# Kernel optimization log

Hardware: AMD Instinct MI355X
Metric: run time of the kernel (lower is better)

## Reference

```python
import jax, jax.numpy as jnp
import numpy as np

D_MODEL = 1024
N_HEAD = 16
HEAD_DIM = D_MODEL // N_HEAD
BS, SEQ = 4, 2048
NEG_INF = -1e9


def setup_inputs() -> dict:
    key = jax.random.key(0)
    ks = jax.random.split(key, 10)
    X = jax.random.normal(ks[0], (BS, SEQ, D_MODEL), dtype=jnp.float32)
    kpm = jax.random.randint(ks[1], (BS, SEQ), 0, 2, dtype=jnp.int32)
    kpm = kpm.at[:, 0].set(0)  # guarantee at least one attendable key per batch
    scale = 1.0 / np.sqrt(D_MODEL)
    WQ = jax.random.normal(ks[2], (D_MODEL, D_MODEL), dtype=jnp.float32) * scale
    bQ = jnp.zeros((D_MODEL,), dtype=jnp.float32)
    WK = jax.random.normal(ks[3], (D_MODEL, D_MODEL), dtype=jnp.float32) * scale
    bK = jnp.zeros((D_MODEL,), dtype=jnp.float32)
    WV = jax.random.normal(ks[4], (D_MODEL, D_MODEL), dtype=jnp.float32) * scale
    bV = jnp.zeros((D_MODEL,), dtype=jnp.float32)
    WO = jax.random.normal(ks[5], (D_MODEL, D_MODEL), dtype=jnp.float32) * scale
    bO = jnp.zeros((D_MODEL,), dtype=jnp.float32)
    return {"X": X, "key_padding_mask": kpm, "WQ": WQ, "bQ": bQ,
            "WK": WK, "bK": bK, "WV": WV, "bV": bV, "WO": WO, "bO": bO}


def reference(X, key_padding_mask, WQ, bQ, WK, bK, WV, bV, WO, bO):
    bs, L, _ = X.shape
    # separate Q/K/V linear projections (torch Linear: x @ W.T + b)
    Q = X @ WQ.T + bQ
    K = X @ WK.T + bK
    V = X @ WV.T + bV
    # split heads: (bs, L, H, Dh) -> (bs, H, L, Dh)
    Q = Q.reshape(bs, L, N_HEAD, HEAD_DIM).transpose(0, 2, 1, 3)
    K = K.reshape(bs, L, N_HEAD, HEAD_DIM).transpose(0, 2, 1, 3)
    V = V.reshape(bs, L, N_HEAD, HEAD_DIM).transpose(0, 2, 1, 3)
    # scaled dot-product attention
    scores = jnp.einsum('bhqd,bhkd->bhqk', Q, K) / jnp.sqrt(
        jnp.asarray(HEAD_DIM, dtype=Q.dtype))
    # key padding mask: non-zero => ignore that key
    mask = (key_padding_mask != 0)[:, None, None, :]  # (bs,1,1,L)
    scores = jnp.where(mask, NEG_INF, scores)
    attn = jax.nn.softmax(scores, axis=-1)
    out = jnp.einsum('bhqk,bhkd->bhqd', attn, V)
    # merge heads
    out = out.transpose(0, 2, 1, 3).reshape(bs, L, D_MODEL)
    return out @ WO.T + bO
```

## Files before the change

kernel.cpp:

```cpp
#include <hip/hip_runtime.h>
#include <stdint.h>

#define BS_   4
#define SEQ_  2048
#define DM_   1024
#define NH_   16
#define DH_   64
#define MTOK_ (BS_*SEQ_)

typedef __attribute__((ext_vector_type(8))) short bf16x8;
typedef __attribute__((ext_vector_type(4))) float f32x4;

__device__ __forceinline__ unsigned short f2bf(float f) {
    union { float f; uint32_t u; } v; v.f = f;
    uint32_t r = v.u + 0x7fffu + ((v.u >> 16) & 1u);
    return (unsigned short)(r >> 16);
}

__device__ __forceinline__ float fexp2(float x) {
#if __has_builtin(__builtin_amdgcn_exp2f)
    return __builtin_amdgcn_exp2f(x);
#else
    return __expf(x * 0.69314718055994531f);
#endif
}

__device__ __forceinline__ uint32_t cvt_pk_bf16(float lo, float hi) {
    uint32_t r;
    asm("v_cvt_pk_bf16_f32 %0, %1, %2" : "=v"(r) : "v"(lo), "v"(hi));
    return r;
}

__device__ __forceinline__ void gload_lds16(const void* g, void* l) {
    __builtin_amdgcn_global_load_lds(
        (const __attribute__((address_space(1))) void*)g,
        (__attribute__((address_space(3))) void*)l, 16, 0, 0);
}

__global__ void cvt_kernel(const float* __restrict__ src,
                           unsigned short* __restrict__ dst, int n) {
    int i = (blockIdx.x * blockDim.x + threadIdx.x) * 4;
    const int stride = gridDim.x * blockDim.x * 4;
    for (; i < n; i += stride) {
        float4 v = *(const float4*)(src + i);
        ushort4 o;
        o.x = f2bf(v.x); o.y = f2bf(v.y); o.z = f2bf(v.z); o.w = f2bf(v.w);
        *(ushort4*)(dst + i) = o;
    }
}

template<int MODE>
__global__ __launch_bounds__(256) void gemm_bt(
    const unsigned short* __restrict__ A,
    const unsigned short* __restrict__ B,
    int Ndim, int Kdim,
    const float* __restrict__ bias0,
    const float* __restrict__ bias1,
    const float* __restrict__ bias2,
    unsigned short* __restrict__ Qo,
    unsigned short* __restrict__ Ko,
    unsigned short* __restrict__ Vt,
    float* __restrict__ Co)
{
    __shared__ unsigned short As[128 * 32];
    __shared__ unsigned short Bs[128 * 32];

    const int t    = threadIdx.x;
    const int lane = t & 63;
    const int w    = t >> 6;
    const int wr   = w >> 1, wc = w & 1;
    const int g    = lane >> 4, li = lane & 15;

    const int ntile = Ndim >> 7;
    const int tm = blockIdx.x / ntile;
    const int tn = blockIdx.x % ntile;

    const unsigned short* Ab = A + (size_t)tm * 128 * Kdim;
    const unsigned short* Bb = B + (size_t)tn * 128 * Kdim;

    f32x4 acc[4][4];
    const f32x4 zero = {0.f, 0.f, 0.f, 0.f};
    #pragma unroll
    for (int i = 0; i < 4; ++i)
        #pragma unroll
        for (int j = 0; j < 4; ++j)
            acc[i][j] = zero;

    const int s0 = t, s1 = t + 256;
    const int r0 = s0 >> 2, c0 = (s0 & 3) << 3;
    const int r1 = s1 >> 2, c1 = (s1 & 3) << 3;

    for (int k0 = 0; k0 < Kdim; k0 += 32) {
        gload_lds16(Ab + (size_t)r0 * Kdim + k0 + c0, (char*)As + s0 * 16);
        gload_lds16(Ab + (size_t)r1 * Kdim + k0 + c1, (char*)As + s1 * 16);
        gload_lds16(Bb + (size_t)r0 * Kdim + k0 + c0, (char*)Bs + s0 * 16);
        gload_lds16(Bb + (size_t)r1 * Kdim + k0 + c1, (char*)Bs + s1 * 16);
        __syncthreads();

        bf16x8 a[4], b[4];
        #pragma unroll
        for (int mi = 0; mi < 4; ++mi)
            a[mi] = *(const bf16x8*)&As[(wr * 64 + mi * 16 + li) * 32 + g * 8];
        #pragma unroll
        for (int ni = 0; ni < 4; ++ni)
            b[ni] = *(const bf16x8*)&Bs[(wc * 64 + ni * 16 + li) * 32 + g * 8];

        #pragma unroll
        for (int mi = 0; mi < 4; ++mi)
            #pragma unroll
            for (int ni = 0; ni < 4; ++ni)
                acc[mi][ni] = __builtin_amdgcn_mfma_f32_16x16x32_bf16(
                    a[mi], b[ni], acc[mi][ni], 0, 0, 0);
        __syncthreads();
    }

    if constexpr (MODE == 0) {
        #pragma unroll
        for (int mi = 0; mi < 4; ++mi) {
            const int gm0 = tm * 128 + wr * 64 + mi * 16 + g * 4;
            const int bb  = gm0 >> 11;
            const int l0  = gm0 & (SEQ_ - 1);
            #pragma unroll
            for (int ni = 0; ni < 4; ++ni) {
                const int gn  = tn * 128 + wc * 64 + ni * 16 + li;
                const int mat = gn >> 10;
                const int c   = gn & (DM_ - 1);
                const int hh  = c >> 6;
                const int dd  = c & (DH_ - 1);
                const float bias = (mat == 0 ? bias0 : (mat == 1 ? bias1 : bias2))[c];
                const f32x4 v = acc[mi][ni];
                if (mat == 2) {
                    ushort4 o;
                    o.x = f2bf(v[0] + bias);
                    o.y = f2bf(v[1] + bias);
                    o.z = f2bf(v[2] + bias);
                    o.w = f2bf(v[3] + bias);
                    *(ushort4*)&Vt[((size_t)(bb * NH_ + hh) * DH_ + dd) * SEQ_ + l0] = o;
                } else {
                    unsigned short* dst = (mat == 0) ? Qo : Ko;
                    #pragma unroll
                    for (int r = 0; r < 4; ++r)
                        dst[((size_t)(bb * NH_ + hh) * SEQ_ + l0 + r) * DH_ + dd] =
                            f2bf(v[r] + bias);
                }
            }
        }
    } else {
        #pragma unroll
        for (int mi = 0; mi < 4; ++mi) {
            const int gm0 = tm * 128 + wr * 64 + mi * 16 + g * 4;
            #pragma unroll
            for (int ni = 0; ni < 4; ++ni) {
                const int gn = tn * 128 + wc * 64 + ni * 16 + li;
                const float bias = bias0[gn];
                #pragma unroll
                for (int r = 0; r < 4; ++r)
                    Co[(size_t)(gm0 + r) * Ndim + gn] = acc[mi][ni][r] + bias;
            }
        }
    }
}

#define KPAD 72

__global__ __launch_bounds__(256) void attn_kernel(
    const unsigned short* __restrict__ Q,
    const unsigned short* __restrict__ K,
    const unsigned short* __restrict__ Vt,
    const int* __restrict__ kpm,
    unsigned short* __restrict__ Oo)
{
    __shared__ unsigned short Ks[64 * KPAD];
    __shared__ unsigned short Vs[64 * KPAD];
    __shared__ float maskLds[64];

    const int t    = threadIdx.x;
    const int lane = t & 63;
    const int w    = t >> 6;
    const int g    = lane >> 4, li = lane & 15;

    const int bh = blockIdx.x >> 4;
    const int qt = blockIdx.x & 15;
    const int b  = bh >> 4;
    const int h  = bh & 15;
    const int q0 = qt * 128 + w * 32;

    bf16x8 qf[2][2];
    #pragma unroll
    for (int qi = 0; qi < 2; ++qi)
        #pragma unroll
        for (int kk = 0; kk < 2; ++kk)
            qf[qi][kk] = *(const bf16x8*)&Q[((size_t)bh * SEQ_ + q0 + qi * 16 + li) * DH_
                                            + kk * 32 + g * 8];

    f32x4 Oacc[2][4];
    const f32x4 zero = {0.f, 0.f, 0.f, 0.f};
    #pragma unroll
    for (int qi = 0; qi < 2; ++qi)
        #pragma unroll
        for (int di = 0; di < 4; ++di)
            Oacc[qi][di] = zero;

    float mrun[2] = {-1e30f, -1e30f};
    float lrun[2] = {0.f, 0.f};

    const int sr = t >> 3;
    const int sc = (t & 7) * 8;

    bf16x8 kreg0, kreg1, vreg0, vreg1;
    float mreg = 0.f;

    auto load_tile = [&](int kv) {
        kreg0 = *(const bf16x8*)&K[((size_t)bh * SEQ_ + kv + sr) * DH_ + sc];
        kreg1 = *(const bf16x8*)&K[((size_t)bh * SEQ_ + kv + sr + 32) * DH_ + sc];
        vreg0 = *(const bf16x8*)&Vt[((size_t)bh * DH_ + sr) * SEQ_ + kv + sc];
        vreg1 = *(const bf16x8*)&Vt[((size_t)bh * DH_ + sr + 32) * SEQ_ + kv + sc];
        if (t < 64) mreg = kpm[b * SEQ_ + kv + t] ? -1e9f : 0.0f;
    };
    auto store_tile = [&]() {
        *(bf16x8*)&Ks[sr * KPAD + sc] = kreg0;
        *(bf16x8*)&Ks[(sr + 32) * KPAD + sc] = kreg1;
        *(bf16x8*)&Vs[sr * KPAD + sc] = vreg0;
        *(bf16x8*)&Vs[(sr + 32) * KPAD + sc] = vreg1;
        if (t < 64) maskLds[t] = mreg;
    };

    load_tile(0);
    store_tile();

    const float SA = 0.18033688011112042f;

    for (int kv = 0; kv < SEQ_; kv += 64) {
        __syncthreads();
        const bool more = (kv + 64) < SEQ_;
        if (more) load_tile(kv + 64);

        float4 mk[4];
        #pragma unroll
        for (int ni = 0; ni < 4; ++ni)
            mk[ni] = *(const float4*)&maskLds[ni * 16 + g * 4];

        f32x4 sacc[2][4];
        #pragma unroll
        for (int qi = 0; qi < 2; ++qi)
            #pragma unroll
            for (int ni = 0; ni < 4; ++ni)
                sacc[qi][ni] = zero;
        #pragma unroll
        for (int ni = 0; ni < 4; ++ni) {
            #pragma unroll
            for (int kk = 0; kk < 2; ++kk) {
                bf16x8 kb = *(const bf16x8*)&Ks[(ni * 16 + li) * KPAD + kk * 32 + g * 8];
                sacc[0][ni] = __builtin_amdgcn_mfma_f32_16x16x32_bf16(
                    kb, qf[0][kk], sacc[0][ni], 0, 0, 0);
                sacc[1][ni] = __builtin_amdgcn_mfma_f32_16x16x32_bf16(
                    kb, qf[1][kk], sacc[1][ni], 0, 0, 0);
            }
        }

        #pragma unroll
        for (int qi = 0; qi < 2; ++qi)
            #pragma unroll
            for (int ni = 0; ni < 4; ++ni) {
                sacc[qi][ni][0] = sacc[qi][ni][0] * SA + mk[ni].x;
                sacc[qi][ni][1] = sacc[qi][ni][1] * SA + mk[ni].y;
                sacc[qi][ni][2] = sacc[qi][ni][2] * SA + mk[ni].z;
                sacc[qi][ni][3] = sacc[qi][ni][3] * SA + mk[ni].w;
            }

        #pragma unroll
        for (int qi = 0; qi < 2; ++qi) {
            float pm = sacc[qi][0][0];
            #pragma unroll
            for (int ni = 0; ni < 4; ++ni)
                #pragma unroll
                for (int r = 0; r < 4; ++r)
                    pm = fmaxf(pm, sacc[qi][ni][r]);
            pm = fmaxf(pm, __shfl_xor(pm, 16));
            pm = fmaxf(pm, __shfl_xor(pm, 32));
            if (!__all(pm <= mrun[qi] + 8.0f)) {
                const float mnew = fmaxf(mrun[qi], pm);
                const float scl  = fexp2(mrun[qi] - mnew);
                mrun[qi] = mnew;
                lrun[qi] *= scl;
                #pragma unroll
                for (int di = 0; di < 4; ++di)
                    #pragma unroll
                    for (int r = 0; r < 4; ++r)
                        Oacc[qi][di][r] *= scl;
            }
            float rs = 0.f;
            #pragma unroll
            for (int ni = 0; ni < 4; ++ni)
                #pragma unroll
                for (int r = 0; r < 4; ++r) {
                    const float p = fexp2(sacc[qi][ni][r] - mrun[qi]);
                    sacc[qi][ni][r] = p;
                    rs += p;
                }
            rs += __shfl_xor(rs, 16);
            rs += __shfl_xor(rs, 32);
            lrun[qi] += rs;
        }

        bf16x8 pa[2][2];
        #pragma unroll
        for (int qi = 0; qi < 2; ++qi)
            #pragma unroll
            for (int kk = 0; kk < 2; ++kk) {
                union { bf16x8 v; uint32_t w4[4]; } u;
                u.w4[0] = cvt_pk_bf16(sacc[qi][2 * kk][0],     sacc[qi][2 * kk][1]);
                u.w4[1] = cvt_pk_bf16(sacc[qi][2 * kk][2],     sacc[qi][2 * kk][3]);
                u.w4[2] = cvt_pk_bf16(sacc[qi][2 * kk + 1][0], sacc[qi][2 * kk + 1][1]);
                u.w4[3] = cvt_pk_bf16(sacc[qi][2 * kk + 1][2], sacc[qi][2 * kk + 1][3]);
                pa[qi][kk] = u.v;
            }

        #pragma unroll
        for (int di = 0; di < 4; ++di) {
            #pragma unroll
            for (int kk = 0; kk < 2; ++kk) {
                union { bf16x8 v; ushort4 h[2]; } uv;
                uv.h[0] = *(const ushort4*)&Vs[(di * 16 + li) * KPAD + kk * 32 + g * 4];
                uv.h[1] = *(const ushort4*)&Vs[(di * 16 + li) * KPAD + kk * 32 + 16 + g * 4];
                Oacc[0][di] = __builtin_amdgcn_mfma_f32_16x16x32_bf16(
                    uv.v, pa[0][kk], Oacc[0][di], 0, 0, 0);
                Oacc[1][di] = __builtin_amdgcn_mfma_f32_16x16x32_bf16(
                    uv.v, pa[1][kk], Oacc[1][di], 0, 0, 0);
            }
        }

        __syncthreads();
        if (more) store_tile();
    }

    #pragma unroll
    for (int qi = 0; qi < 2; ++qi) {
        const float inv = 1.0f / lrun[qi];
        const int q = q0 + qi * 16 + li;
        #pragma unroll
        for (int di = 0; di < 4; ++di) {
            ushort4 o;
            o.x = f2bf(Oacc[qi][di][0] * inv);
            o.y = f2bf(Oacc[qi][di][1] * inv);
            o.z = f2bf(Oacc[qi][di][2] * inv);
            o.w = f2bf(Oacc[qi][di][3] * inv);
            *(ushort4*)&Oo[((size_t)b * SEQ_ + q) * DM_ + h * 64 + di * 16 + g * 4] = o;
        }
    }
}

extern "C" void kernel_launch(void* const* d_in, const int* in_sizes, int n_in,
                              void* d_out, int out_size, void* d_ws, size_t ws_size,
                              hipStream_t stream) {
    const float* X  = (const float*)d_in[0];
    const int*  kpm = (const int*)d_in[1];
    const float* WQ = (const float*)d_in[2];
    const float* bQ = (const float*)d_in[3];
    const float* WK = (const float*)d_in[4];
    const float* bK = (const float*)d_in[5];
    const float* WV = (const float*)d_in[6];
    const float* bV = (const float*)d_in[7];
    const float* WO = (const float*)d_in[8];
    const float* bO = (const float*)d_in[9];
    float* Out = (float*)d_out;

    char* ws = (char*)d_ws;
    unsigned short* Xb  = (unsigned short*)(ws);
    unsigned short* Wb  = (unsigned short*)(ws + (16u << 20));
    unsigned short* WOb = (unsigned short*)(ws + (22u << 20));
    unsigned short* Qb  = (unsigned short*)(ws + (24u << 20));
    unsigned short* Kb  = (unsigned short*)(ws + (40u << 20));
    unsigned short* Vtb = (unsigned short*)(ws + (56u << 20));
    unsigned short* AOb = Xb;

    cvt_kernel<<<2048, 256, 0, stream>>>(X,  Xb,                 (int)(MTOK_ * DM_));
    cvt_kernel<<<1024, 256, 0, stream>>>(WQ, Wb,                 DM_ * DM_);
    cvt_kernel<<<1024, 256, 0, stream>>>(WK, Wb + DM_ * DM_,     DM_ * DM_);
    cvt_kernel<<<1024, 256, 0, stream>>>(WV, Wb + 2 * DM_ * DM_, DM_ * DM_);
    cvt_kernel<<<1024, 256, 0, stream>>>(WO, WOb,                DM_ * DM_);

    gemm_bt<0><<<(MTOK_ / 128) * (3 * DM_ / 128), 256, 0, stream>>>(
        Xb, Wb, 3 * DM_, DM_, bQ, bK, bV, Qb, Kb, Vtb, nullptr);

    attn_kernel<<<BS_ * NH_ * (SEQ_ / 128), 256, 0, stream>>>(Qb, Kb, Vtb, kpm, AOb);

    gemm_bt<1><<<(MTOK_ / 128) * (DM_ / 128), 256, 0, stream>>>(
        AOb, WOb, DM_, DM_, bO, nullptr, nullptr, nullptr, nullptr, nullptr, Out);
}
```

Baseline: 253.0 us.

## Fuse weight conversions, swizzle GEMM tiles, raise MFMA priority, defer row-sum reduction

Merges the four weight fp32-to-bf16 conversions into one launch writing a contiguous buffer. Remaps GEMM block indices so consecutive tiles are spread across the 8 XCDs, for better L2 locality. In attention, wraps the MFMA loops in s_setprio, builds the row max as a balanced tree, and accumulates per-lane partial row sums, doing the cross-lane reduction once at the end instead of every KV tile. Together these cut launch count, shuffles and dependency chains, at the cost of code relying on fixed matrix sizes and the workspace layout.

After: 250.9 us. No clear change (-0.8%).

```diff
diff --git a/kernel.cpp b/kernel.cpp
--- a/kernel.cpp
+++ b/kernel.cpp
@@ -10,6 +10,8 @@
 
 typedef __attribute__((ext_vector_type(8))) short bf16x8;
 typedef __attribute__((ext_vector_type(4))) float f32x4;
+
+#define SA_ 0.18033688011112042f
 
 __device__ __forceinline__ unsigned short f2bf(float f) {
     union { float f; uint32_t u; } v; v.f = f;
@@ -47,6 +49,19 @@
         o.x = f2bf(v.x); o.y = f2bf(v.y); o.z = f2bf(v.z); o.w = f2bf(v.w);
         *(ushort4*)(dst + i) = o;
     }
+}
+
+__global__ void cvt4_kernel(const float* __restrict__ s0, const float* __restrict__ s1,
+                            const float* __restrict__ s2, const float* __restrict__ s3,
+                            unsigned short* __restrict__ dst) {
+    const int i = (blockIdx.x * blockDim.x + threadIdx.x) * 4;
+    const int mat = i >> 20;
+    const int off = i & ((1 << 20) - 1);
+    const float* s = (mat == 0) ? s0 : (mat == 1) ? s1 : (mat == 2) ? s2 : s3;
+    float4 v = *(const float4*)(s + off);
+    ushort4 o;
+    o.x = f2bf(v.x); o.y = f2bf(v.y); o.z = f2bf(v.z); o.w = f2bf(v.w);
+    *(ushort4*)(dst + i) = o;
 }
 
 template<int MODE>
@@ -72,8 +87,10 @@
     const int g    = lane >> 4, li = lane & 15;
 
     const int ntile = Ndim >> 7;
-    const int tm = blockIdx.x / ntile;
-    const int tn = blockIdx.x % ntile;
+    const int per   = gridDim.x >> 3;
+    const int sw    = (blockIdx.x & 7) * per + (blockIdx.x >> 3);
+    const int tm = sw / ntile;
+    const int tn = sw % ntile;
 
     const unsigned short* Ab = A + (size_t)tm * 128 * Kdim;
     const unsigned short* Bb = B + (size_t)tn * 128 * Kdim;
@@ -228,8 +245,6 @@
     load_tile(0);
     store_tile();
 
-    const float SA = 0.18033688011112042f;
-
     for (int kv = 0; kv < SEQ_; kv += 64) {
         __syncthreads();
         const bool more = (kv + 64) < SEQ_;
@@ -246,6 +261,7 @@
             #pragma unroll
             for (int ni = 0; ni < 4; ++ni)
                 sacc[qi][ni] = zero;
+        __builtin_amdgcn_s_setprio(1);
         #pragma unroll
         for (int ni = 0; ni < 4; ++ni) {
             #pragma unroll
@@ -257,25 +273,29 @@
                     kb, qf[1][kk], sacc[1][ni], 0, 0, 0);
             }
         }
+        __builtin_amdgcn_s_setprio(0);
 
         #pragma unroll
         for (int qi = 0; qi < 2; ++qi)
             #pragma unroll
             for (int ni = 0; ni < 4; ++ni) {
-                sacc[qi][ni][0] = sacc[qi][ni][0] * SA + mk[ni].x;
-                sacc[qi][ni][1] = sacc[qi][ni][1] * SA + mk[ni].y;
-                sacc[qi][ni][2] = sacc[qi][ni][2] * SA + mk[ni].z;
-                sacc[qi][ni][3] = sacc[qi][ni][3] * SA + mk[ni].w;
+                sacc[qi][ni][0] = sacc[qi][ni][0] * SA_ + mk[ni].x;
+                sacc[qi][ni][1] = sacc[qi][ni][1] * SA_ + mk[ni].y;
+                sacc[qi][ni][2] = sacc[qi][ni][2] * SA_ + mk[ni].z;
+                sacc[qi][ni][3] = sacc[qi][ni][3] * SA_ + mk[ni].w;
             }
 
         #pragma unroll
         for (int qi = 0; qi < 2; ++qi) {
-            float pm = sacc[qi][0][0];
-            #pragma unroll
-            for (int ni = 0; ni < 4; ++ni)
-                #pragma unroll
-                for (int r = 0; r < 4; ++r)
-                    pm = fmaxf(pm, sacc[qi][ni][r]);
+            float pa0 = fmaxf(fmaxf(sacc[qi][0][0], sacc[qi][0][1]),
+                              fmaxf(sacc[qi][0][2], sacc[qi][0][3]));
+            float pa1 = fmaxf(fmaxf(sacc[qi][1][0], sacc[qi][1][1]),
+                              fmaxf(sacc[qi][1][2], sacc[qi][1][3]));
+            float pa2 = fmaxf(fmaxf(sacc[qi][2][0], sacc[qi][2][1]),
+                              fmaxf(sacc[qi][2][2], sacc[qi][2][3]));
+            float pa3 = fmaxf(fmaxf(sacc[qi][3][0], sacc[qi][3][1]),
+                              fmaxf(sacc[qi][3][2], sacc[qi][3][3]));
+            float pm = fmaxf(fmaxf(pa0, pa1), fmaxf(pa2, pa3));
             pm = fmaxf(pm, __shfl_xor(pm, 16));
             pm = fmaxf(pm, __shfl_xor(pm, 32));
             if (!__all(pm <= mrun[qi] + 8.0f)) {
@@ -298,8 +318,6 @@
                     sacc[qi][ni][r] = p;
                     rs += p;
                 }
-            rs += __shfl_xor(rs, 16);
-            rs += __shfl_xor(rs, 32);
             lrun[qi] += rs;
         }
 
@@ -316,6 +334,7 @@
                 pa[qi][kk] = u.v;
             }
 
+        __builtin_amdgcn_s_setprio(1);
         #pragma unroll
         for (int di = 0; di < 4; ++di) {
             #pragma unroll
@@ -329,6 +348,7 @@
                     uv.v, pa[1][kk], Oacc[1][di], 0, 0, 0);
             }
         }
+        __builtin_amdgcn_s_setprio(0);
 
         __syncthreads();
         if (more) store_tile();
@@ -336,7 +356,10 @@
 
     #pragma unroll
     for (int qi = 0; qi < 2; ++qi) {
-        const float inv = 1.0f / lrun[qi];
+        float lt = lrun[qi];
+        lt += __shfl_xor(lt, 16);
+        lt += __shfl_xor(lt, 32);
+        const float inv = 1.0f / lt;
         const int q = q0 + qi * 16 + li;
         #pragma unroll
         for (int di = 0; di < 4; ++di) {
@@ -374,11 +397,8 @@
     unsigned short* Vtb = (unsigned short*)(ws + (56u << 20));
     unsigned short* AOb = Xb;
 
-    cvt_kernel<<<2048, 256, 0, stream>>>(X,  Xb,                 (int)(MTOK_ * DM_));
-    cvt_kernel<<<1024, 256, 0, stream>>>(WQ, Wb,                 DM_ * DM_);
-    cvt_kernel<<<1024, 256, 0, stream>>>(WK, Wb + DM_ * DM_,     DM_ * DM_);
-    cvt_kernel<<<1024, 256, 0, stream>>>(WV, Wb + 2 * DM_ * DM_, DM_ * DM_);
-    cvt_kernel<<<1024, 256, 0, stream>>>(WO, WOb,                DM_ * DM_);
+    cvt_kernel<<<2048, 256, 0, stream>>>(X, Xb, (int)(MTOK_ * DM_));
+    cvt4_kernel<<<4096, 256, 0, stream>>>(WQ, WK, WV, WO, Wb);
 
     gemm_bt<0><<<(MTOK_ / 128) * (3 * DM_ / 128), 256, 0, stream>>>(
         Xb, Wb, 3 * DM_, DM_, bQ, bK, bV, Qb, Kb, Vtb, nullptr);
```
